# Kernel optimization log

Measured on AMD Instinct MI355X. Metric: run time of the kernel, lower is better.

## Reference

```python
import jax, jax.numpy as jnp
import numpy as np

K = 3   # spatial_kernel_size
M = 5   # memory_size


def setup_inputs() -> dict:
    key = jax.random.key(0)
    ks = jax.random.split(key, 16)
    C = 64
    B, H, D, W = 2, 24, 24, 24
    s = 0.05
    n = jax.random.normal
    return {
        "x": n(ks[0], (B, C, H, D, W), jnp.float32),
        "prev_memory": jnp.zeros((B, C), jnp.float32),
        "Wq": n(ks[1], (C, C), jnp.float32) * s,
        "bq": n(ks[2], (C,), jnp.float32) * s,
        "Wk": n(ks[3], (C, C), jnp.float32) * s,
        "bk": n(ks[4], (C,), jnp.float32) * s,
        "Wv": n(ks[5], (C, C), jnp.float32) * s,
        "bv": n(ks[6], (C,), jnp.float32) * s,
        "mem_key": n(ks[7], (C, M), jnp.float32),
        "mem_value": n(ks[8], (C, M), jnp.float32),
        "Wg": n(ks[9], (C, 2 * C), jnp.float32) * s,
        "bg": n(ks[10], (C,), jnp.float32) * s,
        "W_ih": n(ks[11], (3 * C, C), jnp.float32) * s,
        "W_hh": n(ks[12], (3 * C, C), jnp.float32) * s,
        "b_ih": n(ks[13], (3 * C,), jnp.float32) * s,
        "b_hh": n(ks[14], (3 * C,), jnp.float32) * s,
    }


def _patches(x, k):
    # x: (B,C,H,D,W) -> (B,C,k^3,H,D,W) local neighborhoods (zero-padded)
    B, C, H, D, W = x.shape
    p = k // 2
    xp = jnp.pad(x, ((0, 0), (0, 0), (p, p), (p, p), (p, p)))
    sl = [xp[:, :, i:i + H, j:j + D, l:l + W]
          for i in range(k) for j in range(k) for l in range(k)]
    return jnp.stack(sl, axis=2)


def reference(x, prev_memory, Wq, bq, Wk, bk, Wv, bv, mem_key, mem_value,
              Wg, bg, W_ih, W_hh, b_ih, b_hh):
    B, C, H, D, W = x.shape
    N = H * D * W
    xf = x.reshape(B, C, N)
    pf = _patches(x, K).reshape(B, C, K ** 3, N)

    # 1x1x1 conv projections (pure channel mixes)
    q = jnp.einsum('oc,bcn->bon', Wq, xf) + bq[None, :, None]            # (B,C,N)
    k_sp = jnp.einsum('oc,bcmn->bomn', Wk, pf) + bk[None, :, None, None]  # (B,C,27,N)
    v_sp = jnp.einsum('oc,bcmn->bomn', Wv, pf) + bv[None, :, None, None]

    # memory tokens broadcast over all spatial locations
    k_mem = jnp.broadcast_to(mem_key[None, :, :, None], (B, C, M, N))
    v_mem = jnp.broadcast_to(mem_value[None, :, :, None], (B, C, M, N))
    kk = jnp.concatenate([k_mem, k_sp], axis=2)   # (B,C,M+27,N)
    vv = jnp.concatenate([v_mem, v_sp], axis=2)

    # per-channel scalar attention over memory+neighborhood axis
    attn = jax.nn.softmax(q[:, :, None, :] * kk / jnp.sqrt(jnp.float32(C)), axis=2)
    out = jnp.sum(attn * vv, axis=2).reshape(B, C, H, D, W)

    # sigmoid gate over concat([x, out])
    gin = jnp.concatenate([xf, out.reshape(B, C, N)], axis=1)  # (B,2C,N)
    gate = jax.nn.sigmoid(jnp.einsum('oc,bcn->bon', Wg, gin)
                          + bg[None, :, None]).reshape(B, C, H, D, W)
    out = gate * out + (1.0 - gate) * x

    # GRU memory update on spatially pooled features (torch GRUCell math)
    mu = out.mean(axis=(2, 3, 4))                 # (B,C)
    gi = mu @ W_ih.T + b_ih
    gh = prev_memory @ W_hh.T + b_hh
    ir, iz, ii = jnp.split(gi, 3, axis=1)
    hr, hz, hn = jnp.split(gh, 3, axis=1)
    r = jax.nn.sigmoid(ir + hr)
    z = jax.nn.sigmoid(iz + hz)
    ng = jnp.tanh(ii + r * hn)
    new_memory = (1.0 - z) * ng + z * prev_memory
    return out, new_memory
```

## Files before the change

### kernel.cpp

```cpp
#include <hip/hip_runtime.h>
#include <math.h>

#define NPOS 13824
#define CDIM 64
#define BTCH 2
#define LOG2E 1.4426950408889634f
#define QSCALE (0.125f * LOG2E)

__device__ __forceinline__ unsigned int f2bf1(float f) {
  unsigned int u = __float_as_uint(f);
  return (u + 0x7FFFu + ((u >> 16) & 1u)) >> 16;
}

__global__ __launch_bounds__(256) void qkvg_kernel(
    const float* __restrict__ x,
    const float* __restrict__ Wq, const float* __restrict__ bq,
    const float* __restrict__ Wk, const float* __restrict__ bk,
    const float* __restrict__ Wv, const float* __restrict__ bv,
    const float* __restrict__ Wg,
    float* __restrict__ Qb, unsigned int* __restrict__ KVp,
    float* __restrict__ GXT, float* __restrict__ pool)
{
  __shared__ __align__(16) float wqt[64*68];
  __shared__ __align__(16) float wkt[64*68];
  __shared__ __align__(16) float wvt[64*68];
  __shared__ __align__(16) float wgt[64*68];
  const int t  = threadIdx.x;
  const int bi = blockIdx.x;
  const int b  = bi / 216;
  const int n0 = (bi - b*216) * 64;
  if (bi == 0 && t < 128) pool[t] = 0.0f;

  #pragma unroll
  for (int k = 0; k < 16; ++k) {
    int idx = t + k*256;
    int lo = idx & 63, hi = idx >> 6;
    wqt[lo*68 + hi] = Wq[idx] * QSCALE;
    wkt[lo*68 + hi] = Wk[idx];
    wvt[lo*68 + hi] = Wv[idx];
    wgt[lo*68 + hi] = Wg[hi*128 + lo];
  }
  __syncthreads();

  const int c0  = (t & 15) * 4;
  const int nn0 = (t >> 4) * 4;
  const float* xbase = x + (size_t)(b*64)*NPOS + n0 + nn0;
  float aq[4][4] = {}; float ak[4][4] = {}; float av[4][4] = {}; float ag[4][4] = {};
  #pragma unroll 4
  for (int cp = 0; cp < 64; ++cp) {
    const float4 xv4 = *(const float4*)(xbase + (size_t)cp*NPOS);
    const float4 q4  = *(const float4*)&wqt[cp*68 + c0];
    const float4 k4  = *(const float4*)&wkt[cp*68 + c0];
    const float4 v4  = *(const float4*)&wvt[cp*68 + c0];
    const float4 g4  = *(const float4*)&wgt[cp*68 + c0];
    const float xa[4] = {xv4.x, xv4.y, xv4.z, xv4.w};
    const float qa[4] = {q4.x, q4.y, q4.z, q4.w};
    const float ka[4] = {k4.x, k4.y, k4.z, k4.w};
    const float va[4] = {v4.x, v4.y, v4.z, v4.w};
    const float ga[4] = {g4.x, g4.y, g4.z, g4.w};
    #pragma unroll
    for (int ci = 0; ci < 4; ++ci)
      #pragma unroll
      for (int ni = 0; ni < 4; ++ni) {
        aq[ci][ni] = fmaf(qa[ci], xa[ni], aq[ci][ni]);
        ak[ci][ni] = fmaf(ka[ci], xa[ni], ak[ci][ni]);
        av[ci][ni] = fmaf(va[ci], xa[ni], av[ci][ni]);
        ag[ci][ni] = fmaf(ga[ci], xa[ni], ag[ci][ni]);
      }
  }
  float4 xr[4];
  #pragma unroll
  for (int e = 0; e < 4; ++e)
    xr[e] = *(const float4*)(x + (size_t)(b*64 + c0 + e)*NPOS + n0 + nn0);
  const float xre[4][4] = {{xr[0].x,xr[0].y,xr[0].z,xr[0].w},
                           {xr[1].x,xr[1].y,xr[1].z,xr[1].w},
                           {xr[2].x,xr[2].y,xr[2].z,xr[2].w},
                           {xr[3].x,xr[3].y,xr[3].z,xr[3].w}};
  const float4 bq4 = *(const float4*)&bq[c0];
  const float4 bk4 = *(const float4*)&bk[c0];
  const float4 bv4 = *(const float4*)&bv[c0];
  #pragma unroll
  for (int ni = 0; ni < 4; ++ni) {
    const int p = b*NPOS + n0 + nn0 + ni;
    float4 o;
    o = make_float4(fmaf(bq4.x,QSCALE,aq[0][ni]), fmaf(bq4.y,QSCALE,aq[1][ni]),
                    fmaf(bq4.z,QSCALE,aq[2][ni]), fmaf(bq4.w,QSCALE,aq[3][ni]));
    *(float4*)&Qb[p*64 + c0] = o;
    uint4 kv;
    kv.x = (f2bf1(ak[0][ni]+bk4.x) << 16) | f2bf1(av[0][ni]+bv4.x);
    kv.y = (f2bf1(ak[1][ni]+bk4.y) << 16) | f2bf1(av[1][ni]+bv4.y);
    kv.z = (f2bf1(ak[2][ni]+bk4.z) << 16) | f2bf1(av[2][ni]+bv4.z);
    kv.w = (f2bf1(ak[3][ni]+bk4.w) << 16) | f2bf1(av[3][ni]+bv4.w);
    *(uint4*)&KVp[p*64 + c0] = kv;
    o = make_float4(ag[0][ni], xre[0][ni], ag[1][ni], xre[1][ni]);
    *(float4*)&GXT[(size_t)(p*64 + c0)*2]     = o;
    o = make_float4(ag[2][ni], xre[2][ni], ag[3][ni], xre[3][ni]);
    *(float4*)&GXT[(size_t)(p*64 + c0)*2 + 4] = o;
  }
}

__global__ __launch_bounds__(256, 4) void attn_kernel(
    float* __restrict__ QOT,
    const unsigned int* __restrict__ KVp,
    const float* __restrict__ GXT,
    const float* __restrict__ bk, const float* __restrict__ bv,
    const float* __restrict__ memk, const float* __restrict__ memv,
    const float* __restrict__ Wg, const float* __restrict__ bg,
    float* __restrict__ pool)
{
  __shared__ __align__(16) unsigned int kvbuf[8000];
  __shared__ __align__(16) float alsA[256];
  __shared__ __align__(16) float alsB[256];
  const int t = threadIdx.x;
  const int c = t & 63;
  const int w = t >> 6;

  {
    float* wgt2 = (float*)kvbuf;
    #pragma unroll
    for (int k = 0; k < 16; ++k) {
      int u = t + k*256;
      int cp = u >> 6, j = u & 63;
      wgt2[j*65 + cp] = Wg[cp*128 + 64 + j];
    }
  }
  __syncthreads();
  unsigned int wg2p[32];
  {
    const float* wgt2 = (const float*)kvbuf;
    #pragma unroll
    for (int j2 = 0; j2 < 32; ++j2) {
      unsigned lo = f2bf1(wgt2[(2*j2)*65 + c]);
      unsigned hi = f2bf1(wgt2[(2*j2+1)*65 + c]);
      wg2p[j2] = lo | (hi << 16);
    }
  }
  float mk[5], mv[5];
  #pragma unroll
  for (int m = 0; m < 5; ++m) { mk[m] = memk[c*5 + m]; mv[m] = memv[c*5 + m]; }
  const float bg_c = bg[c];
  __syncthreads();

  const int bi = (int)(blockIdx.x & 7) * 128 + (int)(blockIdx.x >> 3);
  const int b  = bi >> 9;
  const int tb = bi & 511;
  const int h0 = (tb >> 6) * 3;
  const int d0 = ((tb >> 3) & 7) * 3;
  const int w0 = (tb & 7) * 3;
  const int bN = b * NPOS;

  for (int u = t; u < 125*16; u += 256) {
    int pos = u >> 4, q4 = u & 15;
    int ph = pos / 25, pr = pos - ph*25;
    int pd = pr / 5,  pw = pr - pd*5;
    int hh = h0 - 1 + ph, dd = d0 - 1 + pd, ww = w0 - 1 + pw;
    bool inb = ((unsigned)hh < 24u) && ((unsigned)dd < 24u) && ((unsigned)ww < 24u);
    uint4 kv;
    if (inb) {
      kv = *(const uint4*)(KVp + ((size_t)(bN + hh*576 + dd*24 + ww))*64 + q4*4);
    } else {
      const float4 kf = ((const float4*)bk)[q4];
      const float4 vf = ((const float4*)bv)[q4];
      kv.x = (f2bf1(kf.x) << 16) | f2bf1(vf.x);
      kv.y = (f2bf1(kf.y) << 16) | f2bf1(vf.y);
      kv.z = (f2bf1(kf.z) << 16) | f2bf1(vf.z);
      kv.w = (f2bf1(kf.w) << 16) | f2bf1(vf.w);
    }
    *(uint4*)&kvbuf[pos*64 + q4*4] = kv;
  }
  __syncthreads();

  float pacc = 0.0f;
  for (int li = w; li < 27; li += 8) {
    const int liB0 = li + 4;
    const bool hasB = liB0 < 27;
    const int liB = hasB ? liB0 : li;

    const int lhA = li / 9,  lrA = li - lhA*9;
    const int ldA = lrA / 3, lwA = lrA - ldA*3;
    const int pA  = bN + (h0+lhA)*576 + (d0+ldA)*24 + (w0+lwA);
    const int hbA = (lhA*25 + ldA*5 + lwA)*64 + c;
    const int lhB = liB / 9,  lrB = liB - lhB*9;
    const int ldB = lrB / 3,  lwB = lrB - ldB*3;
    const int pB  = bN + (h0+lhB)*576 + (d0+ldB)*24 + (w0+lwB);
    const int hbB = (lhB*25 + ldB*5 + lwB)*64 + c;

    const float qA = QOT[pA*64 + c];
    const float qB = QOT[pB*64 + c];
    const float2 gxA = *(const float2*)&GXT[(size_t)(pA*64 + c)*2];
    const float2 gxB = *(const float2*)&GXT[(size_t)(pB*64 + c)*2];

    float sA0 = 0.f, sA1 = 0.f, oA0 = 0.f, oA1 = 0.f;
    float sB0 = 0.f, sB1 = 0.f, oB0 = 0.f, oB1 = 0.f;
    #pragma unroll
    for (int m = 0; m < 5; ++m) {
      const float pfA = __builtin_amdgcn_exp2f(qA * mk[m]);
      const float pfB = __builtin_amdgcn_exp2f(qB * mk[m]);
      if (m & 1) { sA1 += pfA; oA1 = fmaf(pfA, mv[m], oA1);
                   sB1 += pfB; oB1 = fmaf(pfB, mv[m], oB1); }
      else       { sA0 += pfA; oA0 = fmaf(pfA, mv[m], oA0);
                   sB0 += pfB; oB0 = fmaf(pfB, mv[m], oB0); }
    }
    const unsigned int* kvA = &kvbuf[hbA];
    const unsigned int* kvB = &kvbuf[hbB];
    #pragma unroll
    for (int i = 0; i < 3; ++i)
      #pragma unroll
      for (int j = 0; j < 3; ++j)
        #pragma unroll
        for (int l = 0; l < 3; ++l) {
          const int s4  = i*9 + j*3 + l;
          const int off = (i*25 + j*5 + l)*64;
          const unsigned a = kvA[off], bb2 = kvB[off];
          const float kA = __uint_as_float(a & 0xFFFF0000u);
          const float vA = __uint_as_float(a << 16);
          const float kB = __uint_as_float(bb2 & 0xFFFF0000u);
          const float vB = __uint_as_float(bb2 << 16);
          const float pfA = __builtin_amdgcn_exp2f(qA * kA);
          const float pfB = __builtin_amdgcn_exp2f(qB * kB);
          if (s4 & 1) { sA1 += pfA; oA1 = fmaf(pfA, vA, oA1);
                        sB1 += pfB; oB1 = fmaf(pfB, vB, oB1); }
          else        { sA0 += pfA; oA0 = fmaf(pfA, vA, oA0);
                        sB0 += pfB; oB0 = fmaf(pfB, vB, oB0); }
        }
    const float attA = (oA0 + oA1) * __builtin_amdgcn_rcpf(sA0 + sA1);
    const float attB = (oB0 + oB1) * __builtin_amdgcn_rcpf(sB0 + sB1);

    alsA[w*64 + c] = attA;
    alsB[w*64 + c] = attB;
    float gA0 = gxA.x + bg_c, gA1 = 0.f, gA2 = 0.f, gA3 = 0.f;
    float gB0 = gxB.x + bg_c, gB1 = 0.f, gB2 = 0.f, gB3 = 0.f;
    #pragma unroll
    for (int j4 = 0; j4 < 16; ++j4) {
      const float4 a4 = *(const float4*)&alsA[w*64 + j4*4];
      const float4 b4 = *(const float4*)&alsB[w*64 + j4*4];
      const unsigned pk0 = wg2p[2*j4], pk1 = wg2p[2*j4+1];
      const float w0f = __uint_as_float(pk0 << 16);
      const float w1f = __uint_as_float(pk0 & 0xFFFF0000u);
      const float w2f = __uint_as_float(pk1 << 16);
      const float w3f = __uint_as_float(pk1 & 0xFFFF0000u);
      gA0 = fmaf(w0f, a4.x, gA0); gB0 = fmaf(w0f, b4.x, gB0);
      gA1 = fmaf(w1f, a4.y, gA1); gB1 = fmaf(w1f, b4.y, gB1);
      gA2 = fmaf(w2f, a4.z, gA2); gB2 = fmaf(w2f, b4.z, gB2);
      gA3 = fmaf(w3f, a4.w, gA3); gB3 = fmaf(w3f, b4.w, gB3);
    }
    const float glA   = (gA0 + gA1) + (gA2 + gA3);
    const float glB   = (gB0 + gB1) + (gB2 + gB3);
    const float gateA = __builtin_amdgcn_rcpf(1.0f + __builtin_amdgcn_exp2f(-LOG2E * glA));
    const float gateB = __builtin_amdgcn_rcpf(1.0f + __builtin_amdgcn_exp2f(-LOG2E * glB));
    const float finA  = fmaf(gateA, attA - gxA.y, gxA.y);
    const float finB  = fmaf(gateB, attB - gxB.y, gxB.y);
    QOT[pA*64 + c] = finA;
    pacc += finA;
    if (hasB) { QOT[pB*64 + c] = finB; pacc += finB; }
  }

  alsA[t] = pacc;
  __syncthreads();
  if (t < 64) {
    float s = alsA[t] + alsA[64 + t] + alsA[128 + t] + alsA[192 + t];
    atomicAdd(&pool[b*64 + t], s);
  }
}

__global__ __launch_bounds__(256) void outpool_kernel(
    const float* __restrict__ OT, float* __restrict__ out,
    const float* __restrict__ pool, const float* __restrict__ prev,
    const float* __restrict__ W_ih, const float* __restrict__ W_hh,
    const float* __restrict__ b_ih, const float* __restrict__ b_hh,
    float* __restrict__ outmem)
{
  __shared__ __align__(16) float ls[64*65];
  __shared__ __align__(16) float mu[128];
  __shared__ float gi[384];
  __shared__ float gh[384];
  const int t  = threadIdx.x;
  const int bi = blockIdx.x;
  const int b  = bi / 216;
  const int n0 = (bi - b*216) * 64;
  #pragma unroll
  for (int i = 0; i < 16; ++i) {
    int u = i*256 + t;
    int pos = u >> 6, cc = u & 63;
    ls[cc*65 + pos] = OT[(size_t)(b*NPOS + n0 + pos)*64 + cc];
  }
  if (bi == 0 && t < 128) mu[t] = pool[t] * (1.0f / (float)NPOS);
  __syncthreads();
  #pragma unroll
  for (int i = 0; i < 16; ++i) {
    int u = i*256 + t;
    int cc = u >> 6, j = u & 63;
    out[(size_t)(b*64 + cc)*NPOS + n0 + j] = ls[cc*65 + j];
  }
  if (bi != 0) return;

  for (int r = t; r < 384; r += 256) {
    const int b2 = r / 192, j = r - b2*192;
    const float4* wi4 = (const float4*)(W_ih + (size_t)j*64);
    const float4* wh4 = (const float4*)(W_hh + (size_t)j*64);
    const float4* mu4 = (const float4*)(mu + b2*64);
    const float4* pv4 = (const float4*)(prev + b2*64);
    float sgi = b_ih[j], sgh = b_hh[j];
    #pragma unroll
    for (int k = 0; k < 16; ++k) {
      float4 wv = wi4[k], m4 = mu4[k];
      sgi = fmaf(wv.x, m4.x, sgi); sgi = fmaf(wv.y, m4.y, sgi);
      sgi = fmaf(wv.z, m4.z, sgi); sgi = fmaf(wv.w, m4.w, sgi);
      float4 hv = wh4[k], p4 = pv4[k];
      sgh = fmaf(hv.x, p4.x, sgh); sgh = fmaf(hv.y, p4.y, sgh);
      sgh = fmaf(hv.z, p4.z, sgh); sgh = fmaf(hv.w, p4.w, sgh);
    }
    gi[r] = sgi; gh[r] = sgh;
  }
  __syncthreads();
  if (t < 128) {
    const int b2 = t >> 6, cc = t & 63;
    float ir = gi[b2*192 + cc],       hr = gh[b2*192 + cc];
    float iz = gi[b2*192 + 64 + cc],  hz = gh[b2*192 + 64 + cc];
    float ii = gi[b2*192 + 128 + cc], hn = gh[b2*192 + 128 + cc];
    float rr = 1.0f / (1.0f + __builtin_amdgcn_exp2f(-LOG2E * (ir + hr)));
    float zz = 1.0f / (1.0f + __builtin_amdgcn_exp2f(-LOG2E * (iz + hz)));
    float ng = tanhf(ii + rr * hn);
    outmem[t] = (1.0f - zz) * ng + zz * prev[t];
  }
}

extern "C" void kernel_launch(void* const* d_in, const int* in_sizes, int n_in,
                              void* d_out, int out_size, void* d_ws, size_t ws_size,
                              hipStream_t stream) {
  const float* x    = (const float*)d_in[0];
  const float* prev = (const float*)d_in[1];
  const float* Wq   = (const float*)d_in[2];
  const float* bq   = (const float*)d_in[3];
  const float* Wk   = (const float*)d_in[4];
  const float* bk   = (const float*)d_in[5];
  const float* Wv   = (const float*)d_in[6];
  const float* bv   = (const float*)d_in[7];
  const float* memk = (const float*)d_in[8];
  const float* memv = (const float*)d_in[9];
  const float* Wg   = (const float*)d_in[10];
  const float* bg   = (const float*)d_in[11];
  const float* W_ih = (const float*)d_in[12];
  const float* W_hh = (const float*)d_in[13];
  const float* b_ih = (const float*)d_in[14];
  const float* b_hh = (const float*)d_in[15];

  float* out    = (float*)d_out;
  float* outmem = out + (size_t)BTCH*CDIM*NPOS;

  const size_t SZ = (size_t)BTCH*NPOS*CDIM;
  float* wsf       = (float*)d_ws;
  float* Qb        = wsf;
  unsigned int* KVp = (unsigned int*)(wsf + SZ);
  float* GXT       = wsf + 2*SZ;
  float* pool      = wsf + 4*SZ;

  qkvg_kernel<<<BTCH*216, 256, 0, stream>>>(x, Wq, bq, Wk, bk, Wv, bv, Wg,
                                            Qb, KVp, GXT, pool);
  attn_kernel<<<BTCH*512, 256, 0, stream>>>(Qb, KVp, GXT,
                                            bk, bv, memk, memv, Wg, bg, pool);
  outpool_kernel<<<BTCH*216, 256, 0, stream>>>(Qb, out, pool, prev,
                                               W_ih, W_hh, b_ih, b_hh, outmem);
}
```

Measured before the change: 150.2 us.

## Pack Q and gate logits as bf16, transpose KV tile, process four positions per warp

The projection kernel now packs the scaled query and gate pre-activation into one bf16 pair stored next to x, so the separate fp32 Q buffer write is dropped and the attention kernel issues one load per position. The attention kernel stores its KV halo tile channel-major with a 129-word stride and fills it with scalar per-channel loads. Each warp now handles up to four output positions per pass instead of two, which adds independent exp work to hide latency. The cost is lower query precision, more register pressure, and less coalesced tile fill loads.

```diff
diff --git a/kernel.cpp b/kernel.cpp
--- a/kernel.cpp
+++ b/kernel.cpp
@@ -18,8 +18,8 @@
     const float* __restrict__ Wk, const float* __restrict__ bk,
     const float* __restrict__ Wv, const float* __restrict__ bv,
     const float* __restrict__ Wg,
-    float* __restrict__ Qb, unsigned int* __restrict__ KVp,
-    float* __restrict__ GXT, float* __restrict__ pool)
+    unsigned int* __restrict__ KVp, float* __restrict__ QGX,
+    float* __restrict__ pool)
 {
   __shared__ __align__(16) float wqt[64*68];
   __shared__ __align__(16) float wkt[64*68];
@@ -79,38 +79,41 @@
   const float4 bq4 = *(const float4*)&bq[c0];
   const float4 bk4 = *(const float4*)&bk[c0];
   const float4 bv4 = *(const float4*)&bv[c0];
+  const float bqa[4] = {bq4.x, bq4.y, bq4.z, bq4.w};
+  const float bka[4] = {bk4.x, bk4.y, bk4.z, bk4.w};
+  const float bva[4] = {bv4.x, bv4.y, bv4.z, bv4.w};
   #pragma unroll
   for (int ni = 0; ni < 4; ++ni) {
     const int p = b*NPOS + n0 + nn0 + ni;
+    uint4 kv;
+    kv.x = (f2bf1(ak[0][ni]+bka[0]) << 16) | f2bf1(av[0][ni]+bva[0]);
+    kv.y = (f2bf1(ak[1][ni]+bka[1]) << 16) | f2bf1(av[1][ni]+bva[1]);
+    kv.z = (f2bf1(ak[2][ni]+bka[2]) << 16) | f2bf1(av[2][ni]+bva[2]);
+    kv.w = (f2bf1(ak[3][ni]+bka[3]) << 16) | f2bf1(av[3][ni]+bva[3]);
+    *(uint4*)&KVp[p*64 + c0] = kv;
+    unsigned pk0 = (f2bf1(fmaf(bqa[0], QSCALE, aq[0][ni])) << 16) | f2bf1(ag[0][ni]);
+    unsigned pk1 = (f2bf1(fmaf(bqa[1], QSCALE, aq[1][ni])) << 16) | f2bf1(ag[1][ni]);
+    unsigned pk2 = (f2bf1(fmaf(bqa[2], QSCALE, aq[2][ni])) << 16) | f2bf1(ag[2][ni]);
+    unsigned pk3 = (f2bf1(fmaf(bqa[3], QSCALE, aq[3][ni])) << 16) | f2bf1(ag[3][ni]);
     float4 o;
-    o = make_float4(fmaf(bq4.x,QSCALE,aq[0][ni]), fmaf(bq4.y,QSCALE,aq[1][ni]),
-                    fmaf(bq4.z,QSCALE,aq[2][ni]), fmaf(bq4.w,QSCALE,aq[3][ni]));
-    *(float4*)&Qb[p*64 + c0] = o;
-    uint4 kv;
-    kv.x = (f2bf1(ak[0][ni]+bk4.x) << 16) | f2bf1(av[0][ni]+bv4.x);
-    kv.y = (f2bf1(ak[1][ni]+bk4.y) << 16) | f2bf1(av[1][ni]+bv4.y);
-    kv.z = (f2bf1(ak[2][ni]+bk4.z) << 16) | f2bf1(av[2][ni]+bv4.z);
-    kv.w = (f2bf1(ak[3][ni]+bk4.w) << 16) | f2bf1(av[3][ni]+bv4.w);
-    *(uint4*)&KVp[p*64 + c0] = kv;
-    o = make_float4(ag[0][ni], xre[0][ni], ag[1][ni], xre[1][ni]);
-    *(float4*)&GXT[(size_t)(p*64 + c0)*2]     = o;
-    o = make_float4(ag[2][ni], xre[2][ni], ag[3][ni], xre[3][ni]);
-    *(float4*)&GXT[(size_t)(p*64 + c0)*2 + 4] = o;
+    o = make_float4(__uint_as_float(pk0), xre[0][ni], __uint_as_float(pk1), xre[1][ni]);
+    *(float4*)&QGX[(size_t)(p*64 + c0)*2]     = o;
+    o = make_float4(__uint_as_float(pk2), xre[2][ni], __uint_as_float(pk3), xre[3][ni]);
+    *(float4*)&QGX[(size_t)(p*64 + c0)*2 + 4] = o;
   }
 }
 
 __global__ __launch_bounds__(256, 4) void attn_kernel(
-    float* __restrict__ QOT,
+    float* __restrict__ OT,
     const unsigned int* __restrict__ KVp,
-    const float* __restrict__ GXT,
+    const float* __restrict__ QGX,
     const float* __restrict__ bk, const float* __restrict__ bv,
     const float* __restrict__ memk, const float* __restrict__ memv,
     const float* __restrict__ Wg, const float* __restrict__ bg,
     float* __restrict__ pool)
 {
-  __shared__ __align__(16) unsigned int kvbuf[8000];
-  __shared__ __align__(16) float alsA[256];
-  __shared__ __align__(16) float alsB[256];
+  __shared__ __align__(16) unsigned int kvbuf[64*129];
+  __shared__ __align__(16) float als[4][256];
   const int t = threadIdx.x;
   const int c = t & 63;
   const int w = t >> 6;
@@ -139,6 +142,7 @@
   #pragma unroll
   for (int m = 0; m < 5; ++m) { mk[m] = memk[c*5 + m]; mv[m] = memv[c*5 + m]; }
   const float bg_c = bg[c];
+  const unsigned bias_kv = (f2bf1(bk[c]) << 16) | f2bf1(bv[c]);
   __syncthreads();
 
   const int bi = (int)(blockIdx.x & 7) * 128 + (int)(blockIdx.x >> 3);
@@ -149,60 +153,49 @@
   const int w0 = (tb & 7) * 3;
   const int bN = b * NPOS;
 
-  for (int u = t; u < 125*16; u += 256) {
-    int pos = u >> 4, q4 = u & 15;
-    int ph = pos / 25, pr = pos - ph*25;
-    int pd = pr / 5,  pw = pr - pd*5;
-    int hh = h0 - 1 + ph, dd = d0 - 1 + pd, ww = w0 - 1 + pw;
-    bool inb = ((unsigned)hh < 24u) && ((unsigned)dd < 24u) && ((unsigned)ww < 24u);
-    uint4 kv;
-    if (inb) {
-      kv = *(const uint4*)(KVp + ((size_t)(bN + hh*576 + dd*24 + ww))*64 + q4*4);
-    } else {
-      const float4 kf = ((const float4*)bk)[q4];
-      const float4 vf = ((const float4*)bv)[q4];
-      kv.x = (f2bf1(kf.x) << 16) | f2bf1(vf.x);
-      kv.y = (f2bf1(kf.y) << 16) | f2bf1(vf.y);
-      kv.z = (f2bf1(kf.z) << 16) | f2bf1(vf.z);
-      kv.w = (f2bf1(kf.w) << 16) | f2bf1(vf.w);
-    }
-    *(uint4*)&kvbuf[pos*64 + q4*4] = kv;
+  for (int u = t; u < 8000; u += 256) {
+    const int pos = u >> 6;
+    const int ph = pos / 25, pr = pos - ph*25;
+    const int pd = pr / 5,  pw = pr - pd*5;
+    const int hh = h0 - 1 + ph, dd = d0 - 1 + pd, ww = w0 - 1 + pw;
+    const bool inb = ((unsigned)hh < 24u) && ((unsigned)dd < 24u) && ((unsigned)ww < 24u);
+    unsigned kv = bias_kv;
+    if (inb) kv = KVp[(size_t)(bN + hh*576 + dd*24 + ww)*64 + c];
+    kvbuf[c*129 + pos] = kv;
   }
   __syncthreads();
 
   float pacc = 0.0f;
-  for (int li = w; li < 27; li += 8) {
-    const int liB0 = li + 4;
-    const bool hasB = liB0 < 27;
-    const int liB = hasB ? liB0 : li;
-
-    const int lhA = li / 9,  lrA = li - lhA*9;
-    const int ldA = lrA / 3, lwA = lrA - ldA*3;
-    const int pA  = bN + (h0+lhA)*576 + (d0+ldA)*24 + (w0+lwA);
-    const int hbA = (lhA*25 + ldA*5 + lwA)*64 + c;
-    const int lhB = liB / 9,  lrB = liB - lhB*9;
-    const int ldB = lrB / 3,  lwB = lrB - ldB*3;
-    const int pB  = bN + (h0+lhB)*576 + (d0+ldB)*24 + (w0+lwB);
-    const int hbB = (lhB*25 + ldB*5 + lwB)*64 + c;
-
-    const float qA = QOT[pA*64 + c];
-    const float qB = QOT[pB*64 + c];
-    const float2 gxA = *(const float2*)&GXT[(size_t)(pA*64 + c)*2];
-    const float2 gxB = *(const float2*)&GXT[(size_t)(pB*64 + c)*2];
-
-    float sA0 = 0.f, sA1 = 0.f, oA0 = 0.f, oA1 = 0.f;
-    float sB0 = 0.f, sB1 = 0.f, oB0 = 0.f, oB1 = 0.f;
-    #pragma unroll
-    for (int m = 0; m < 5; ++m) {
-      const float pfA = __builtin_amdgcn_exp2f(qA * mk[m]);
-      const float pfB = __builtin_amdgcn_exp2f(qB * mk[m]);
-      if (m & 1) { sA1 += pfA; oA1 = fmaf(pfA, mv[m], oA1);
-                   sB1 += pfB; oB1 = fmaf(pfB, mv[m], oB1); }
-      else       { sA0 += pfA; oA0 = fmaf(pfA, mv[m], oA0);
-                   sB0 += pfB; oB0 = fmaf(pfB, mv[m], oB0); }
-    }
-    const unsigned int* kvA = &kvbuf[hbA];
-    const unsigned int* kvB = &kvbuf[hbB];
+  #pragma unroll
+  for (int half = 0; half < 2; ++half) {
+    const int li0 = w + half*16;
+    bool val[4]; int p[4]; const unsigned int* kvrow[4];
+    float q2[4], gxl[4], xv[4];
+    #pragma unroll
+    for (int s = 0; s < 4; ++s) {
+      int li = li0 + 4*s;
+      val[s] = li < 27;
+      if (!val[s]) li = li0;
+      const int lh = li / 9, lr = li - lh*9;
+      const int ld = lr / 3, lw = lr - ld*3;
+      p[s]     = bN + (h0+lh)*576 + (d0+ld)*24 + (w0+lw);
+      kvrow[s] = &kvbuf[c*129 + lh*25 + ld*5 + lw];
+      const float2 gq = *(const float2*)&QGX[(size_t)(p[s]*64 + c)*2];
+      const unsigned uq = __float_as_uint(gq.x);
+      q2[s]  = __uint_as_float(uq & 0xFFFF0000u);
+      gxl[s] = __uint_as_float(uq << 16);
+      xv[s]  = gq.y;
+    }
+
+    float s0[4] = {}, s1[4] = {}, o0[4] = {}, o1[4] = {};
+    #pragma unroll
+    for (int m = 0; m < 5; ++m)
+      #pragma unroll
+      for (int s = 0; s < 4; ++s) {
+        const float pf = __builtin_amdgcn_exp2f(q2[s] * mk[m]);
+        if (m & 1) { s1[s] += pf; o1[s] = fmaf(pf, mv[m], o1[s]); }
+        else       { s0[s] += pf; o0[s] = fmaf(pf, mv[m], o0[s]); }
+      }
     #pragma unroll
     for (int i = 0; i < 3; ++i)
       #pragma unroll
@@ -210,55 +203,59 @@
         #pragma unroll
         for (int l = 0; l < 3; ++l) {
           const int s4  = i*9 + j*3 + l;
-          const int off = (i*25 + j*5 + l)*64;
-          const unsigned a = kvA[off], bb2 = kvB[off];
-          const float kA = __uint_as_float(a & 0xFFFF0000u);
-          const float vA = __uint_as_float(a << 16);
-          const float kB = __uint_as_float(bb2 & 0xFFFF0000u);
-          const float vB = __uint_as_float(bb2 << 16);
-          const float pfA = __builtin_amdgcn_exp2f(qA * kA);
-          const float pfB = __builtin_amdgcn_exp2f(qB * kB);
-          if (s4 & 1) { sA1 += pfA; oA1 = fmaf(pfA, vA, oA1);
-                        sB1 += pfB; oB1 = fmaf(pfB, vB, oB1); }
-          else        { sA0 += pfA; oA0 = fmaf(pfA, vA, oA0);
-                        sB0 += pfB; oB0 = fmaf(pfB, vB, oB0); }
+          const int off = i*25 + j*5 + l;
+          #pragma unroll
+          for (int s = 0; s < 4; ++s) {
+            const unsigned kv = kvrow[s][off];
+            const float kf = __uint_as_float(kv & 0xFFFF0000u);
+            const float vf = __uint_as_float(kv << 16);
+            const float pf = __builtin_amdgcn_exp2f(q2[s] * kf);
+            if (s4 & 1) { s1[s] += pf; o1[s] = fmaf(pf, vf, o1[s]); }
+            else        { s0[s] += pf; o0[s] = fmaf(pf, vf, o0[s]); }
+          }
         }
-    const float attA = (oA0 + oA1) * __builtin_amdgcn_rcpf(sA0 + sA1);
-    const float attB = (oB0 + oB1) * __builtin_amdgcn_rcpf(sB0 + sB1);
-
-    alsA[w*64 + c] = attA;
-    alsB[w*64 + c] = attB;
-    float gA0 = gxA.x + bg_c, gA1 = 0.f, gA2 = 0.f, gA3 = 0.f;
-    float gB0 = gxB.x + bg_c, gB1 = 0.f, gB2 = 0.f, gB3 = 0.f;
+    float att[4];
+    #pragma unroll
+    for (int s = 0; s < 4; ++s) {
+      att[s] = (o0[s] + o1[s]) * __builtin_amdgcn_rcpf(s0[s] + s1[s]);
+      als[s][w*64 + c] = att[s];
+    }
+
+    float g0[4], g1[4] = {}, g2[4] = {}, g3[4] = {};
+    #pragma unroll
+    for (int s = 0; s < 4; ++s) g0[s] = gxl[s] + bg_c;
     #pragma unroll
     for (int j4 = 0; j4 < 16; ++j4) {
-      const float4 a4 = *(const float4*)&alsA[w*64 + j4*4];
-      const float4 b4 = *(const float4*)&alsB[w*64 + j4*4];
       const unsigned pk0 = wg2p[2*j4], pk1 = wg2p[2*j4+1];
       const float w0f = __uint_as_float(pk0 << 16);
       const float w1f = __uint_as_float(pk0 & 0xFFFF0000u);
       const float w2f = __uint_as_float(pk1 << 16);
       const float w3f = __uint_as_float(pk1 & 0xFFFF0000u);
-      gA0 = fmaf(w0f, a4.x, gA0); gB0 = fmaf(w0f, b4.x, gB0);
-      gA1 = fmaf(w1f, a4.y, gA1); gB1 = fmaf(w1f, b4.y, gB1);
-      gA2 = fmaf(w2f, a4.z, gA2); gB2 = fmaf(w2f, b4.z, gB2);
-      gA3 = fmaf(w3f, a4.w, gA3); gB3 = fmaf(w3f, b4.w, gB3);
-    }
-    const float glA   = (gA0 + gA1) + (gA2 + gA3);
-    const float glB   = (gB0 + gB1) + (gB2 + gB3);
-    const float gateA = __builtin_amdgcn_rcpf(1.0f + __builtin_amdgcn_exp2f(-LOG2E * glA));
-    const float gateB = __builtin_amdgcn_rcpf(1.0f + __builtin_amdgcn_exp2f(-LOG2E * glB));
-    const float finA  = fmaf(gateA, attA - gxA.y, gxA.y);
-    const float finB  = fmaf(gateB, attB - gxB.y, gxB.y);
-    QOT[pA*64 + c] = finA;
-    pacc += finA;
-    if (hasB) { QOT[pB*64 + c] = finB; pacc += finB; }
-  }
-
-  alsA[t] = pacc;
+      #pragma unroll
+      for (int s = 0; s < 4; ++s) {
+        const float4 a4 = *(const float4*)&als[s][w*64 + j4*4];
+        g0[s] = fmaf(w0f, a4.x, g0[s]);
+        g1[s] = fmaf(w1f, a4.y, g1[s]);
+        g2[s] = fmaf(w2f, a4.z, g2[s]);
+        g3[s] = fmaf(w3f, a4.w, g3[s]);
+      }
+    }
+    #pragma unroll
+    for (int s = 0; s < 4; ++s) {
+      const float gl   = (g0[s] + g1[s]) + (g2[s] + g3[s]);
+      const float gate = __builtin_amdgcn_rcpf(1.0f + __builtin_amdgcn_exp2f(-LOG2E * gl));
+      const float fin  = fmaf(gate, att[s] - xv[s], xv[s]);
+      if (val[s]) {
+        OT[p[s]*64 + c] = fin;
+        pacc += fin;
+      }
+    }
+  }
+
+  als[0][t] = pacc;
   __syncthreads();
   if (t < 64) {
-    float s = alsA[t] + alsA[64 + t] + alsA[128 + t] + alsA[192 + t];
+    float s = als[0][t] + als[0][64 + t] + als[0][128 + t] + als[0][192 + t];
     atomicAdd(&pool[b*64 + t], s);
   }
 }
@@ -349,16 +346,16 @@
   float* outmem = out + (size_t)BTCH*CDIM*NPOS;
 
   const size_t SZ = (size_t)BTCH*NPOS*CDIM;
-  float* wsf       = (float*)d_ws;
-  float* Qb        = wsf;
+  float* wsf        = (float*)d_ws;
+  float* OT         = wsf;
   unsigned int* KVp = (unsigned int*)(wsf + SZ);
-  float* GXT       = wsf + 2*SZ;
-  float* pool      = wsf + 4*SZ;
+  float* QGX        = wsf + 2*SZ;
+  float* pool       = wsf + 4*SZ;
 
   qkvg_kernel<<<BTCH*216, 256, 0, stream>>>(x, Wq, bq, Wk, bk, Wv, bv, Wg,
-                                            Qb, KVp, GXT, pool);
-  attn_kernel<<<BTCH*512, 256, 0, stream>>>(Qb, KVp, GXT,
+                                            KVp, QGX, pool);
+  attn_kernel<<<BTCH*512, 256, 0, stream>>>(OT, KVp, QGX,
                                             bk, bv, memk, memv, Wg, bg, pool);
-  outpool_kernel<<<BTCH*216, 256, 0, stream>>>(Qb, out, pool, prev,
+  outpool_kernel<<<BTCH*216, 256, 0, stream>>>(OT, out, pool, prev,
                                                W_ih, W_hh, b_ih, b_hh, outmem);
 }
```

Result: slower. 243.0 us (+61.8%).

## Pack Q and gate logits into bf16 alongside x and transpose KV shared tile

Applied to the files above, without the earlier changes.

The QKV projection kernel now packs the scaled query and the gate partial into one bf16 pair stored next to x, so it no longer writes a separate fp32 Q buffer. The attention kernel reads that single interleaved stream instead of two. The shared-memory KV halo tile is rewritten channel-major with a padded stride of 129, loading one word per thread instead of uint4s, which changes the LDS access pattern in the inner loop. Q is now held in bf16, which lowers precision inside the softmax exponent. The halo fill now issues scalar global loads.

```diff
diff --git a/kernel.cpp b/kernel.cpp
--- a/kernel.cpp
+++ b/kernel.cpp
@@ -18,8 +18,8 @@
     const float* __restrict__ Wk, const float* __restrict__ bk,
     const float* __restrict__ Wv, const float* __restrict__ bv,
     const float* __restrict__ Wg,
-    float* __restrict__ Qb, unsigned int* __restrict__ KVp,
-    float* __restrict__ GXT, float* __restrict__ pool)
+    unsigned int* __restrict__ KVp, float* __restrict__ QGX,
+    float* __restrict__ pool)
 {
   __shared__ __align__(16) float wqt[64*68];
   __shared__ __align__(16) float wkt[64*68];
@@ -79,36 +79,40 @@
   const float4 bq4 = *(const float4*)&bq[c0];
   const float4 bk4 = *(const float4*)&bk[c0];
   const float4 bv4 = *(const float4*)&bv[c0];
+  const float bqa[4] = {bq4.x, bq4.y, bq4.z, bq4.w};
+  const float bka[4] = {bk4.x, bk4.y, bk4.z, bk4.w};
+  const float bva[4] = {bv4.x, bv4.y, bv4.z, bv4.w};
   #pragma unroll
   for (int ni = 0; ni < 4; ++ni) {
     const int p = b*NPOS + n0 + nn0 + ni;
+    uint4 kv;
+    kv.x = (f2bf1(ak[0][ni]+bka[0]) << 16) | f2bf1(av[0][ni]+bva[0]);
+    kv.y = (f2bf1(ak[1][ni]+bka[1]) << 16) | f2bf1(av[1][ni]+bva[1]);
+    kv.z = (f2bf1(ak[2][ni]+bka[2]) << 16) | f2bf1(av[2][ni]+bva[2]);
+    kv.w = (f2bf1(ak[3][ni]+bka[3]) << 16) | f2bf1(av[3][ni]+bva[3]);
+    *(uint4*)&KVp[p*64 + c0] = kv;
+    unsigned pk0 = (f2bf1(fmaf(bqa[0], QSCALE, aq[0][ni])) << 16) | f2bf1(ag[0][ni]);
+    unsigned pk1 = (f2bf1(fmaf(bqa[1], QSCALE, aq[1][ni])) << 16) | f2bf1(ag[1][ni]);
+    unsigned pk2 = (f2bf1(fmaf(bqa[2], QSCALE, aq[2][ni])) << 16) | f2bf1(ag[2][ni]);
+    unsigned pk3 = (f2bf1(fmaf(bqa[3], QSCALE, aq[3][ni])) << 16) | f2bf1(ag[3][ni]);
     float4 o;
-    o = make_float4(fmaf(bq4.x,QSCALE,aq[0][ni]), fmaf(bq4.y,QSCALE,aq[1][ni]),
-                    fmaf(bq4.z,QSCALE,aq[2][ni]), fmaf(bq4.w,QSCALE,aq[3][ni]));
-    *(float4*)&Qb[p*64 + c0] = o;
-    uint4 kv;
-    kv.x = (f2bf1(ak[0][ni]+bk4.x) << 16) | f2bf1(av[0][ni]+bv4.x);
-    kv.y = (f2bf1(ak[1][ni]+bk4.y) << 16) | f2bf1(av[1][ni]+bv4.y);
-    kv.z = (f2bf1(ak[2][ni]+bk4.z) << 16) | f2bf1(av[2][ni]+bv4.z);
-    kv.w = (f2bf1(ak[3][ni]+bk4.w) << 16) | f2bf1(av[3][ni]+bv4.w);
-    *(uint4*)&KVp[p*64 + c0] = kv;
-    o = make_float4(ag[0][ni], xre[0][ni], ag[1][ni], xre[1][ni]);
-    *(float4*)&GXT[(size_t)(p*64 + c0)*2]     = o;
-    o = make_float4(ag[2][ni], xre[2][ni], ag[3][ni], xre[3][ni]);
-    *(float4*)&GXT[(size_t)(p*64 + c0)*2 + 4] = o;
+    o = make_float4(__uint_as_float(pk0), xre[0][ni], __uint_as_float(pk1), xre[1][ni]);
+    *(float4*)&QGX[(size_t)(p*64 + c0)*2]     = o;
+    o = make_float4(__uint_as_float(pk2), xre[2][ni], __uint_as_float(pk3), xre[3][ni]);
+    *(float4*)&QGX[(size_t)(p*64 + c0)*2 + 4] = o;
   }
 }
 
 __global__ __launch_bounds__(256, 4) void attn_kernel(
-    float* __restrict__ QOT,
+    float* __restrict__ OT,
     const unsigned int* __restrict__ KVp,
-    const float* __restrict__ GXT,
+    const float* __restrict__ QGX,
     const float* __restrict__ bk, const float* __restrict__ bv,
     const float* __restrict__ memk, const float* __restrict__ memv,
     const float* __restrict__ Wg, const float* __restrict__ bg,
     float* __restrict__ pool)
 {
-  __shared__ __align__(16) unsigned int kvbuf[8000];
+  __shared__ __align__(16) unsigned int kvbuf[64*129];
   __shared__ __align__(16) float alsA[256];
   __shared__ __align__(16) float alsB[256];
   const int t = threadIdx.x;
@@ -139,6 +143,7 @@
   #pragma unroll
   for (int m = 0; m < 5; ++m) { mk[m] = memk[c*5 + m]; mv[m] = memv[c*5 + m]; }
   const float bg_c = bg[c];
+  const unsigned bias_kv = (f2bf1(bk[c]) << 16) | f2bf1(bv[c]);
   __syncthreads();
 
   const int bi = (int)(blockIdx.x & 7) * 128 + (int)(blockIdx.x >> 3);
@@ -149,24 +154,15 @@
   const int w0 = (tb & 7) * 3;
   const int bN = b * NPOS;
 
-  for (int u = t; u < 125*16; u += 256) {
-    int pos = u >> 4, q4 = u & 15;
-    int ph = pos / 25, pr = pos - ph*25;
-    int pd = pr / 5,  pw = pr - pd*5;
-    int hh = h0 - 1 + ph, dd = d0 - 1 + pd, ww = w0 - 1 + pw;
-    bool inb = ((unsigned)hh < 24u) && ((unsigned)dd < 24u) && ((unsigned)ww < 24u);
-    uint4 kv;
-    if (inb) {
-      kv = *(const uint4*)(KVp + ((size_t)(bN + hh*576 + dd*24 + ww))*64 + q4*4);
-    } else {
-      const float4 kf = ((const float4*)bk)[q4];
-      const float4 vf = ((const float4*)bv)[q4];
-      kv.x = (f2bf1(kf.x) << 16) | f2bf1(vf.x);
-      kv.y = (f2bf1(kf.y) << 16) | f2bf1(vf.y);
-      kv.z = (f2bf1(kf.z) << 16) | f2bf1(vf.z);
-      kv.w = (f2bf1(kf.w) << 16) | f2bf1(vf.w);
-    }
-    *(uint4*)&kvbuf[pos*64 + q4*4] = kv;
+  for (int u = t; u < 8000; u += 256) {
+    const int pos = u >> 6;
+    const int ph = pos / 25, pr = pos - ph*25;
+    const int pd = pr / 5,  pw = pr - pd*5;
+    const int hh = h0 - 1 + ph, dd = d0 - 1 + pd, ww = w0 - 1 + pw;
+    const bool inb = ((unsigned)hh < 24u) && ((unsigned)dd < 24u) && ((unsigned)ww < 24u);
+    unsigned kv = bias_kv;
+    if (inb) kv = KVp[(size_t)(bN + hh*576 + dd*24 + ww)*64 + c];
+    kvbuf[c*129 + pos] = kv;
   }
   __syncthreads();
 
@@ -179,16 +175,22 @@
     const int lhA = li / 9,  lrA = li - lhA*9;
     const int ldA = lrA / 3, lwA = lrA - ldA*3;
     const int pA  = bN + (h0+lhA)*576 + (d0+ldA)*24 + (w0+lwA);
-    const int hbA = (lhA*25 + ldA*5 + lwA)*64 + c;
+    const unsigned int* kvA = &kvbuf[c*129 + lhA*25 + ldA*5 + lwA];
     const int lhB = liB / 9,  lrB = liB - lhB*9;
     const int ldB = lrB / 3,  lwB = lrB - ldB*3;
     const int pB  = bN + (h0+lhB)*576 + (d0+ldB)*24 + (w0+lwB);
-    const int hbB = (lhB*25 + ldB*5 + lwB)*64 + c;
-
-    const float qA = QOT[pA*64 + c];
-    const float qB = QOT[pB*64 + c];
-    const float2 gxA = *(const float2*)&GXT[(size_t)(pA*64 + c)*2];
-    const float2 gxB = *(const float2*)&GXT[(size_t)(pB*64 + c)*2];
+    const unsigned int* kvB = &kvbuf[c*129 + lhB*25 + ldB*5 + lwB];
+
+    const float2 gqA = *(const float2*)&QGX[(size_t)(pA*64 + c)*2];
+    const float2 gqB = *(const float2*)&QGX[(size_t)(pB*64 + c)*2];
+    const unsigned uqA = __float_as_uint(gqA.x);
+    const unsigned uqB = __float_as_uint(gqB.x);
+    const float qA  = __uint_as_float(uqA & 0xFFFF0000u);
+    const float gxA = __uint_as_float(uqA << 16);
+    const float xvA = gqA.y;
+    const float qB  = __uint_as_float(uqB & 0xFFFF0000u);
+    const float gxB = __uint_as_float(uqB << 16);
+    const float xvB = gqB.y;
 
     float sA0 = 0.f, sA1 = 0.f, oA0 = 0.f, oA1 = 0.f;
     float sB0 = 0.f, sB1 = 0.f, oB0 = 0.f, oB1 = 0.f;
@@ -201,8 +203,6 @@
       else       { sA0 += pfA; oA0 = fmaf(pfA, mv[m], oA0);
                    sB0 += pfB; oB0 = fmaf(pfB, mv[m], oB0); }
     }
-    const unsigned int* kvA = &kvbuf[hbA];
-    const unsigned int* kvB = &kvbuf[hbB];
     #pragma unroll
     for (int i = 0; i < 3; ++i)
       #pragma unroll
@@ -210,7 +210,7 @@
         #pragma unroll
         for (int l = 0; l < 3; ++l) {
           const int s4  = i*9 + j*3 + l;
-          const int off = (i*25 + j*5 + l)*64;
+          const int off = i*25 + j*5 + l;
           const unsigned a = kvA[off], bb2 = kvB[off];
           const float kA = __uint_as_float(a & 0xFFFF0000u);
           const float vA = __uint_as_float(a << 16);
@@ -228,8 +228,8 @@
 
     alsA[w*64 + c] = attA;
     alsB[w*64 + c] = attB;
-    float gA0 = gxA.x + bg_c, gA1 = 0.f, gA2 = 0.f, gA3 = 0.f;
-    float gB0 = gxB.x + bg_c, gB1 = 0.f, gB2 = 0.f, gB3 = 0.f;
+    float gA0 = gxA + bg_c, gA1 = 0.f, gA2 = 0.f, gA3 = 0.f;
+    float gB0 = gxB + bg_c, gB1 = 0.f, gB2 = 0.f, gB3 = 0.f;
     #pragma unroll
     for (int j4 = 0; j4 < 16; ++j4) {
       const float4 a4 = *(const float4*)&alsA[w*64 + j4*4];
@@ -248,11 +248,11 @@
     const float glB   = (gB0 + gB1) + (gB2 + gB3);
     const float gateA = __builtin_amdgcn_rcpf(1.0f + __builtin_amdgcn_exp2f(-LOG2E * glA));
     const float gateB = __builtin_amdgcn_rcpf(1.0f + __builtin_amdgcn_exp2f(-LOG2E * glB));
-    const float finA  = fmaf(gateA, attA - gxA.y, gxA.y);
-    const float finB  = fmaf(gateB, attB - gxB.y, gxB.y);
-    QOT[pA*64 + c] = finA;
+    const float finA  = fmaf(gateA, attA - xvA, xvA);
+    const float finB  = fmaf(gateB, attB - xvB, xvB);
+    OT[pA*64 + c] = finA;
     pacc += finA;
-    if (hasB) { QOT[pB*64 + c] = finB; pacc += finB; }
+    if (hasB) { OT[pB*64 + c] = finB; pacc += finB; }
   }
 
   alsA[t] = pacc;
@@ -349,16 +349,16 @@
   float* outmem = out + (size_t)BTCH*CDIM*NPOS;
 
   const size_t SZ = (size_t)BTCH*NPOS*CDIM;
-  float* wsf       = (float*)d_ws;
-  float* Qb        = wsf;
+  float* wsf        = (float*)d_ws;
+  float* OT         = wsf;
   unsigned int* KVp = (unsigned int*)(wsf + SZ);
-  float* GXT       = wsf + 2*SZ;
-  float* pool      = wsf + 4*SZ;
+  float* QGX        = wsf + 2*SZ;
+  float* pool       = wsf + 4*SZ;
 
   qkvg_kernel<<<BTCH*216, 256, 0, stream>>>(x, Wq, bq, Wk, bk, Wv, bv, Wg,
-                                            Qb, KVp, GXT, pool);
-  attn_kernel<<<BTCH*512, 256, 0, stream>>>(Qb, KVp, GXT,
+                                            KVp, QGX, pool);
+  attn_kernel<<<BTCH*512, 256, 0, stream>>>(OT, KVp, QGX,
                                             bk, bv, memk, memv, Wg, bg, pool);
-  outpool_kernel<<<BTCH*216, 256, 0, stream>>>(Qb, out, pool, prev,
+  outpool_kernel<<<BTCH*216, 256, 0, stream>>>(OT, out, pool, prev,
                                                W_ih, W_hh, b_ih, b_hh, outmem);
 }
```

Result: slower. 188.7 us (+25.7%).
